# Performance work log

Hardware: AMD Instinct MI355X
Metric: run time of the kernel (lower is better)

The kernel has to match this reference:

```python
import jax, jax.numpy as jnp
import numpy as np

N = 50000      # nodes
E = 800000     # edges
NF = 16        # nfeature_dim
H = 128        # hidden_dim
OUT = 4        # output_dim


def _edge_conv(x, edge_index, W1, b1, W2, b2, aggr):
    """PyG EdgeConv: message = MLP(cat[x_i, x_j - x_i]) per edge, aggregate at target i.
    edge_index[0]=source j, edge_index[1]=target i."""
    src, dst = edge_index[0], edge_index[1]
    xi = x[dst]                                   # [E, F]
    xj = x[src]                                   # [E, F]
    h = jnp.concatenate([xi, xj - xi], axis=-1)   # [E, 2F]
    m = jax.nn.relu(h @ W1 + b1) @ W2 + b2        # [E, H]
    if aggr == 'max':
        out = jax.ops.segment_max(m, dst, num_segments=N)
        out = jnp.where(jnp.isfinite(out), out, 0.0)  # nodes with no in-edges -> 0
    else:  # mean
        s = jax.ops.segment_sum(m, dst, num_segments=N)
        cnt = jax.ops.segment_sum(jnp.ones((m.shape[0], 1), m.dtype), dst, num_segments=N)
        out = s / jnp.maximum(cnt, 1.0)
    return out


def setup_inputs() -> dict:
    key = jax.random.key(0)
    ks = jax.random.split(key, 20)
    s = 0.05
    inp = {
        'x': jax.random.normal(ks[0], (N, NF), dtype=jnp.float32),
        'edge_attr': jax.random.uniform(ks[1], (E, 1), dtype=jnp.float32) + 0.1,
        'edge_index': jax.random.randint(ks[2], (2, E), 0, N, dtype=jnp.int64),
        # conv0: Linear(2*NF->H), Linear(H->H)
        'W01': jax.random.normal(ks[3], (2 * NF, H), dtype=jnp.float32) * s,
        'b01': jnp.zeros((H,), jnp.float32),
        'W02': jax.random.normal(ks[4], (H, H), dtype=jnp.float32) * s,
        'b02': jnp.zeros((H,), jnp.float32),
        # conv1: Linear(2*H->H), Linear(H->H)
        'W11': jax.random.normal(ks[5], (2 * H, H), dtype=jnp.float32) * s,
        'b11': jnp.zeros((H,), jnp.float32),
        'W12': jax.random.normal(ks[6], (H, H), dtype=jnp.float32) * s,
        'b12': jnp.zeros((H,), jnp.float32),
        # conv2: Linear(2*H->H), Linear(H->H)
        'W21': jax.random.normal(ks[7], (2 * H, H), dtype=jnp.float32) * s,
        'b21': jnp.zeros((H,), jnp.float32),
        'W22': jax.random.normal(ks[8], (H, H), dtype=jnp.float32) * s,
        'b22': jnp.zeros((H,), jnp.float32),
        # final fc
        'Wf': jax.random.normal(ks[9], (H, OUT), dtype=jnp.float32) * s,
        'bf': jnp.zeros((OUT,), jnp.float32),
    }
    return inp


def reference(x, edge_attr, edge_index, W01, b01, W02, b02, W11, b11, W12, b12,
              W21, b21, W22, b22, Wf, bf):
    # edge_attr is only nan-checked in the original forward; unused in math.
    # dropout_rate = 0.0 -> identity (eval-mode reference).
    h = _edge_conv(x, edge_index, W01, b01, W02, b02, 'max')
    h = jax.nn.relu(h)
    h = _edge_conv(h, edge_index, W11, b11, W12, b12, 'mean')
    h = jax.nn.relu(h)
    h = _edge_conv(h, edge_index, W21, b21, W22, b22, 'mean')
    return h @ Wf + bf  # [N, OUT]
```

## Files before the change

### kernel.cpp

```cpp
#include <hip/hip_runtime.h>
#include <stdint.h>

#define NNODES 50000
#define NEDGES 800000
#define FDIM 16
#define HDIM 128
#define NPAD 50176
#define NCH 98
#define NBLK64 782

typedef __attribute__((ext_vector_type(8))) short short8;
typedef __attribute__((ext_vector_type(4))) float f32x4;

static constexpr size_t NH  = (size_t)NNODES * HDIM;
static constexpr size_t NHB = NH * sizeof(float);

static constexpr size_t OFF_BUF0  = 0;
static constexpr size_t OFF_BUF1  = NHB;
static constexpr size_t OFF_BUF2  = 2 * NHB;
static constexpr size_t OFF_BFB   = 3 * NHB;
static constexpr size_t OFF_CNT   = OFF_BFB + NH * 2;
static constexpr size_t OFF_CUR   = OFF_CNT + NPAD * 4;
static constexpr size_t OFF_CSUM  = OFF_CUR + NPAD * 4;
static constexpr size_t OFF_COFF  = OFF_CSUM + 512;
static constexpr size_t OFF_WFOLD = OFF_COFF + 512;
static constexpr size_t OFF_BFOLD = OFF_WFOLD + 2048;
static constexpr size_t OFF_FLAG  = OFF_BFOLD + 256;
static constexpr size_t OFF_SEDGE = OFF_FLAG + 256;
static constexpr size_t OFF_W02H  = OFF_SEDGE + (size_t)NEDGES * 8;
static constexpr size_t OFF_W02L  = OFF_W02H + 32768;
static constexpr size_t OFF_W12H  = OFF_W02L + 32768;
static constexpr size_t OFF_W12L  = OFF_W12H + 32768;
static constexpr size_t OFF_W11H  = OFF_W12L + 32768;
static constexpr size_t OFF_W11L  = OFF_W11H + 65536;
static constexpr size_t OFF_W21H  = OFF_W11L + 65536;
static constexpr size_t OFF_W21L  = OFF_W21H + 65536;

__device__ inline unsigned enc_f32(float m) {
  unsigned u = __float_as_uint(m);
  return (u & 0x80000000u) ? ~u : (u | 0x80000000u);
}

__device__ inline ushort bf16_rne(float v) {
  const unsigned u = __float_as_uint(v);
  return (ushort)((u + 0x7fffu + ((u >> 16) & 1u)) >> 16);
}

__device__ inline void bf16_split(float v, ushort& h, ushort& l) {
  unsigned u = __float_as_uint(v);
  unsigned hb = (u + 0x7fffu + ((u >> 16) & 1u)) & 0xffff0000u;
  h = (ushort)(hb >> 16);
  float r = v - __uint_as_float(hb);
  unsigned ur = __float_as_uint(r);
  l = (ushort)((ur + 0x7fffu + ((ur >> 16) & 1u)) >> 16);
}

__device__ inline void split8_tr(const float v[8], short8& hv, short8& lv) {
  unsigned hp[4], lp[4];
  #pragma unroll
  for (int k = 0; k < 4; ++k) {
    const unsigned u0 = __float_as_uint(v[2 * k]);
    const unsigned u1 = __float_as_uint(v[2 * k + 1]);
    const unsigned h0 = u0 & 0xffff0000u;
    const unsigned h1 = u1 & 0xffff0000u;
    const float r0 = v[2 * k]     - __uint_as_float(h0);
    const float r1 = v[2 * k + 1] - __uint_as_float(h1);
    hp[k] = h1 | (h0 >> 16);
    lp[k] = (__float_as_uint(r1) & 0xffff0000u) | (__float_as_uint(r0) >> 16);
  }
  hv = *(short8*)hp;
  lv = *(short8*)lp;
}

__device__ inline short8 cvtpk8_bf16(const float v[8]) {
  unsigned r[4];
  #pragma unroll
  for (int k = 0; k < 4; ++k)
    asm("v_cvt_pk_bf16_f32 %0, %1, %2" : "=v"(r[k]) : "v"(v[2 * k]), "v"(v[2 * k + 1]));
  return *(short8*)r;
}

__global__ __launch_bounds__(256) void k_init(const int* __restrict__ raw,
                                              int* __restrict__ flag,
                                              unsigned* __restrict__ cnt,
                                              unsigned* __restrict__ outenc) {
  const int i = blockIdx.x * 256 + threadIdx.x;
  outenc[i] = 0u;
  if (i < NPAD) cnt[i] = 0u;
  if (i == 0) {
    int is64 = 1;
    #pragma unroll
    for (int k = 1; k < 64; k += 2)
      if (raw[k] != 0) is64 = 0;
    *flag = is64;
  }
}

__global__ __launch_bounds__(256) void k_count(const int* __restrict__ raw,
                                               const int* __restrict__ flag,
                                               unsigned* __restrict__ cnt) {
  const size_t e = (size_t)blockIdx.x * 256 + threadIdx.x;
  const int d = (*flag) ? raw[2 * ((size_t)NEDGES + e)] : raw[NEDGES + e];
  atomicAdd(&cnt[d], 1u);
}

__global__ __launch_bounds__(256) void k_scan1(const unsigned* __restrict__ cnt,
                                               unsigned* __restrict__ csum) {
  __shared__ unsigned s[256];
  const int t = threadIdx.x, b = blockIdx.x;
  s[t] = cnt[b * 512 + t] + cnt[b * 512 + 256 + t];
  __syncthreads();
  for (int off = 128; off; off >>= 1) {
    if (t < off) s[t] += s[t + off];
    __syncthreads();
  }
  if (t == 0) csum[b] = s[0];
}

__global__ void k_scan2(const unsigned* __restrict__ csum,
                        unsigned* __restrict__ coff) {
  if (threadIdx.x == 0) {
    unsigned r = 0;
    for (int i = 0; i < NCH; ++i) { coff[i] = r; r += csum[i]; }
  }
}

__global__ __launch_bounds__(256) void k_scan3(const unsigned* __restrict__ cnt,
                                               const unsigned* __restrict__ coff,
                                               unsigned* __restrict__ cursor) {
  __shared__ unsigned s[256];
  const int t = threadIdx.x, b = blockIdx.x;
  const int base = b * 512;
  const unsigned c0 = cnt[base + 2 * t], c1 = cnt[base + 2 * t + 1];
  s[t] = c0 + c1;
  __syncthreads();
  for (int off = 1; off < 256; off <<= 1) {
    unsigned v = s[t];
    if (t >= off) v += s[t - off];
    __syncthreads();
    s[t] = v;
    __syncthreads();
  }
  const unsigned o = coff[b] + s[t] - (c0 + c1);
  cursor[base + 2 * t] = o;
  cursor[base + 2 * t + 1] = o + c0;
}

__global__ __launch_bounds__(256) void k_scatter(const int* __restrict__ raw,
                                                 const int* __restrict__ flag,
                                                 unsigned* __restrict__ cursor,
                                                 int2* __restrict__ sedge) {
  const size_t e = (size_t)blockIdx.x * 256 + threadIdx.x;
  int s, d;
  if (*flag) { s = raw[2 * e]; d = raw[2 * ((size_t)NEDGES + e)]; }
  else       { s = raw[e];     d = raw[NEDGES + e]; }
  const unsigned p = atomicAdd(&cursor[d], 1u);
  int2 sd; sd.x = s; sd.y = d;
  sedge[p] = sd;
}

__device__ inline void prepw_body(const float* __restrict__ W2,
                                  ushort* __restrict__ Whi,
                                  ushort* __restrict__ Wlo, int blk) {
  const int gid = blk * 256 + threadIdx.x;
  const int row = gid & 15;
  const int kg  = (gid >> 4) & 3;
  const int ks  = (gid >> 6) & 3;
  const int ct  = gid >> 8;
  const int col = ct * 16 + row;
  const int k0  = ks * 32 + kg * 8;
  short8 hv, lv;
  #pragma unroll
  for (int j = 0; j < 8; ++j) {
    ushort h, l;
    bf16_split(W2[(size_t)(k0 + j) * HDIM + col], h, l);
    hv[j] = (short)h; lv[j] = (short)l;
  }
  *(short8*)(Whi + (size_t)gid * 8) = hv;
  *(short8*)(Wlo + (size_t)gid * 8) = lv;
}

__device__ inline void packab_body(const float* __restrict__ W1,
                                   ushort* __restrict__ Whi,
                                   ushort* __restrict__ Wlo, int blk) {
  const int gid = blk * 256 + threadIdx.x;
  const int row = gid & 15;
  const int kg  = (gid >> 4) & 3;
  const int ks  = (gid >> 6) & 3;
  const int ct  = gid >> 8;
  const int col = ct * 16 + row;
  const int k0  = ks * 32 + kg * 8;
  short8 hv, lv;
  #pragma unroll
  for (int j = 0; j < 8; ++j) {
    const int k = k0 + j;
    float v;
    if (col < HDIM) v = W1[(size_t)k * HDIM + col] - W1[(size_t)(k + HDIM) * HDIM + col];
    else            v = W1[(size_t)(k + HDIM) * HDIM + (col - HDIM)];
    ushort h, l;
    bf16_split(v, h, l);
    hv[j] = (short)h; lv[j] = (short)l;
  }
  *(short8*)(Whi + (size_t)gid * 8) = hv;
  *(short8*)(Wlo + (size_t)gid * 8) = lv;
}

__global__ __launch_bounds__(256) void k_prep_all(
    const float* __restrict__ W02, const float* __restrict__ W12,
    const float* __restrict__ W11, const float* __restrict__ W21,
    const float* __restrict__ W22, const float* __restrict__ Wf,
    const float* __restrict__ b22, const float* __restrict__ bf,
    ushort* __restrict__ W02h, ushort* __restrict__ W02l,
    ushort* __restrict__ W12h, ushort* __restrict__ W12l,
    ushort* __restrict__ W11h, ushort* __restrict__ W11l,
    ushort* __restrict__ W21h, ushort* __restrict__ W21l,
    float* __restrict__ Wfold, float* __restrict__ bfold) {
  const int b = blockIdx.x;
  if (b < 8)       prepw_body(W02, W02h, W02l, b);
  else if (b < 16) prepw_body(W12, W12h, W12l, b - 8);
  else if (b < 32) packab_body(W11, W11h, W11l, b - 16);
  else if (b < 48) packab_body(W21, W21h, W21l, b - 32);
  else {
    const int t = (b - 48) * 256 + threadIdx.x;
    const int f = t >> 2, o = t & 3;
    float acc = 0.f;
    for (int h = 0; h < HDIM; ++h)
      acc = fmaf(W22[f * HDIM + h], Wf[h * 4 + o], acc);
    Wfold[t] = acc;
    if (t < 4) {
      float a = bf[t];
      for (int h = 0; h < HDIM; ++h) a = fmaf(b22[h], Wf[h * 4 + t], a);
      bfold[t] = a;
    }
  }
}

__global__ __launch_bounds__(256) void k_node_ab16(const float* __restrict__ x,
                                                   const float* __restrict__ W1,
                                                   const float* __restrict__ b1,
                                                   ushort* __restrict__ Ab,
                                                   ushort* __restrict__ Bb) {
  __shared__ float s_x[16 * FDIM];
  const int tid = threadIdx.x;
  const int nb = blockIdx.x * 16;
  s_x[tid] = x[(size_t)nb * FDIM + tid];
  __syncthreads();
  const int h = tid & 127;
  const int half = tid >> 7;
  float accA[8], accB[8];
  #pragma unroll
  for (int j = 0; j < 8; ++j) { accA[j] = 0.f; accB[j] = 0.f; }
  #pragma unroll 4
  for (int f = 0; f < FDIM; ++f) {
    const float wt = W1[f * HDIM + h];
    const float wb = W1[(f + FDIM) * HDIM + h];
    const float wd = wt - wb;
    #pragma unroll
    for (int j = 0; j < 8; ++j) {
      const float xv = s_x[(half * 8 + j) * FDIM + f];
      accA[j] = fmaf(xv, wd, accA[j]);
      accB[j] = fmaf(xv, wb, accB[j]);
    }
  }
  const float bias = b1[h];
  #pragma unroll
  for (int j = 0; j < 8; ++j) {
    const size_t idx = (size_t)(nb + half * 8 + j) * HDIM + h;
    Ab[idx] = bf16_rne(accA[j] + bias);
    Bb[idx] = bf16_rne(accB[j]);
  }
}

__global__ __launch_bounds__(256) void k_node_ab_mfma(
    const unsigned* __restrict__ X, const ushort* __restrict__ Whi,
    const ushort* __restrict__ Wlo, const float* __restrict__ b1,
    float* __restrict__ A, ushort* __restrict__ Bb) {
  __shared__ __align__(16) ushort s_hi[64 * 128];
  __shared__ __align__(16) ushort s_lo[64 * 128];
  const int tid = threadIdx.x;
  const int nb = blockIdx.x * 64;

  #pragma unroll
  for (int it = 0; it < 4; ++it) {
    const int idx = tid + it * 256;
    const int row = idx >> 4;
    const int kg8 = idx & 15;
    const int n = nb + row;
    float v[8];
    if (n < NNODES) {
      const unsigned* p = X + (size_t)n * HDIM + kg8 * 8;
      const uint4 u0 = *(const uint4*)p;
      const uint4 u1 = *(const uint4*)(p + 4);
      const unsigned uu[8] = {u0.x, u0.y, u0.z, u0.w, u1.x, u1.y, u1.z, u1.w};
      #pragma unroll
      for (int j = 0; j < 8; ++j)
        v[j] = (uu[j] & 0x80000000u) ? __uint_as_float(uu[j] ^ 0x80000000u) : 0.f;
    } else {
      #pragma unroll
      for (int j = 0; j < 8; ++j) v[j] = 0.f;
    }
    short8 hv, lv;
    split8_tr(v, hv, lv);
    const int unit = row * 16 + (kg8 ^ (row & 15));
    *(short8*)(s_hi + unit * 8) = hv;
    *(short8*)(s_lo + unit * 8) = lv;
  }
  __syncthreads();

  const int l15 = tid & 15;
  const int l4  = (tid >> 4) & 3;
  const int w   = tid >> 6;

  f32x4 acc[4][4];
  #pragma unroll
  for (int rt = 0; rt < 4; ++rt)
    #pragma unroll
    for (int c = 0; c < 4; ++c)
      #pragma unroll
      for (int r = 0; r < 4; ++r) acc[rt][c][r] = 0.f;

  #pragma unroll
  for (int ks = 0; ks < 4; ++ks) {
    short8 wh[4], wl[4];
    #pragma unroll
    for (int ctl = 0; ctl < 4; ++ctl) {
      const int ct_g = w * 4 + ctl;
      const size_t u = ((size_t)(((ct_g * 4 + ks) * 4 + l4) * 16 + l15)) * 8;
      wh[ctl] = *(const short8*)(Whi + u);
      wl[ctl] = *(const short8*)(Wlo + u);
    }
    #pragma unroll
    for (int rt = 0; rt < 4; ++rt) {
      const int unit = (rt * 16 + l15) * 16 + ((ks * 4 + l4) ^ l15);
      const short8 ah = *(const short8*)(s_hi + unit * 8);
      const short8 al = *(const short8*)(s_lo + unit * 8);
      #pragma unroll
      for (int ctl = 0; ctl < 4; ++ctl) {
        acc[rt][ctl] = __builtin_amdgcn_mfma_f32_16x16x32_bf16(al, wh[ctl], acc[rt][ctl], 0, 0, 0);
        acc[rt][ctl] = __builtin_amdgcn_mfma_f32_16x16x32_bf16(ah, wl[ctl], acc[rt][ctl], 0, 0, 0);
        acc[rt][ctl] = __builtin_amdgcn_mfma_f32_16x16x32_bf16(ah, wh[ctl], acc[rt][ctl], 0, 0, 0);
      }
    }
  }

  #pragma unroll
  for (int ctl = 0; ctl < 4; ++ctl) {
    const int col_g = w * 64 + ctl * 16 + l15;
    if (col_g < HDIM) {
      const float bias = b1[col_g];
      #pragma unroll
      for (int rt = 0; rt < 4; ++rt)
        #pragma unroll
        for (int r = 0; r < 4; ++r) {
          const int n = nb + rt * 16 + l4 * 4 + r;
          if (n < NNODES) A[(size_t)n * HDIM + col_g] = acc[rt][ctl][r] + bias;
        }
    } else {
      const int cb = col_g - HDIM;
      #pragma unroll
      for (int rt = 0; rt < 4; ++rt)
        #pragma unroll
        for (int r = 0; r < 4; ++r) {
          const int n = nb + rt * 16 + l4 * 4 + r;
          if (n < NNODES) Bb[(size_t)n * HDIM + cb] = bf16_rne(acc[rt][ctl][r]);
        }
    }
  }
}

__global__ __launch_bounds__(256) void k_node_l2_fused(
    const float* __restrict__ S, const unsigned* __restrict__ cnt,
    const ushort* __restrict__ W12h, const ushort* __restrict__ W12l,
    const float* __restrict__ b12,
    const ushort* __restrict__ W21h, const ushort* __restrict__ W21l,
    const float* __restrict__ b21,
    float* __restrict__ A, ushort* __restrict__ Bb) {
  __shared__ __align__(16) ushort s_hi[64 * 128];
  __shared__ __align__(16) ushort s_lo[64 * 128];
  __shared__ float s_m[64 * 132];
  __shared__ float s_scale[64];
  __shared__ float s_alive[64];
  const int tid = threadIdx.x;
  const int nb = blockIdx.x * 64;
  if (tid < 64) {
    const int n = nb + tid;
    const unsigned c = (n < NNODES) ? cnt[n] : 0u;
    s_scale[tid] = c ? 1.f / (float)c : 0.f;
    s_alive[tid] = c ? 1.f : 0.f;
  }
  __syncthreads();

  #pragma unroll
  for (int it = 0; it < 4; ++it) {
    const int idx = tid + it * 256;
    const int row = idx >> 4;
    const int kg8 = idx & 15;
    const int n = nb + row;
    float v[8];
    if (n < NNODES) {
      const float sc = s_scale[row];
      const float* p = S + (size_t)n * HDIM + kg8 * 8;
      const float4 a0 = *(const float4*)p;
      const float4 a1 = *(const float4*)(p + 4);
      v[0] = a0.x * sc; v[1] = a0.y * sc; v[2] = a0.z * sc; v[3] = a0.w * sc;
      v[4] = a1.x * sc; v[5] = a1.y * sc; v[6] = a1.z * sc; v[7] = a1.w * sc;
    } else {
      #pragma unroll
      for (int j = 0; j < 8; ++j) v[j] = 0.f;
    }
    short8 hv, lv;
    split8_tr(v, hv, lv);
    const int unit = row * 16 + (kg8 ^ (row & 15));
    *(short8*)(s_hi + unit * 8) = hv;
    *(short8*)(s_lo + unit * 8) = lv;
  }
  __syncthreads();

  const int l15 = tid & 15;
  const int l4  = (tid >> 4) & 3;
  const int w   = tid >> 6;

  {
    f32x4 acc[4][2];
    #pragma unroll
    for (int rt = 0; rt < 4; ++rt)
      #pragma unroll
      for (int c = 0; c < 2; ++c)
        #pragma unroll
        for (int r = 0; r < 4; ++r) acc[rt][c][r] = 0.f;

    #pragma unroll
    for (int ks = 0; ks < 4; ++ks) {
      short8 wh[2], wl[2];
      #pragma unroll
      for (int ctl = 0; ctl < 2; ++ctl) {
        const int ct_g = w * 2 + ctl;
        const size_t u = ((size_t)(((ct_g * 4 + ks) * 4 + l4) * 16 + l15)) * 8;
        wh[ctl] = *(const short8*)(W12h + u);
        wl[ctl] = *(const short8*)(W12l + u);
      }
      #pragma unroll
      for (int rt = 0; rt < 4; ++rt) {
        const int unit = (rt * 16 + l15) * 16 + ((ks * 4 + l4) ^ l15);
        const short8 ah = *(const short8*)(s_hi + unit * 8);
        const short8 al = *(const short8*)(s_lo + unit * 8);
        #pragma unroll
        for (int ctl = 0; ctl < 2; ++ctl) {
          acc[rt][ctl] = __builtin_amdgcn_mfma_f32_16x16x32_bf16(al, wh[ctl], acc[rt][ctl], 0, 0, 0);
          acc[rt][ctl] = __builtin_amdgcn_mfma_f32_16x16x32_bf16(ah, wl[ctl], acc[rt][ctl], 0, 0, 0);
          acc[rt][ctl] = __builtin_amdgcn_mfma_f32_16x16x32_bf16(ah, wh[ctl], acc[rt][ctl], 0, 0, 0);
        }
      }
    }

    const float bb0 = b12[w * 32 + l15];
    const float bb1 = b12[w * 32 + 16 + l15];
    #pragma unroll
    for (int rt = 0; rt < 4; ++rt)
      #pragma unroll
      for (int ctl = 0; ctl < 2; ++ctl)
        #pragma unroll
        for (int r = 0; r < 4; ++r) {
          const int row = rt * 16 + l4 * 4 + r;
          s_m[row * 132 + w * 32 + ctl * 16 + l15] =
              fmaxf(acc[rt][ctl][r] + (ctl ? bb1 : bb0), 0.f) * s_alive[row];
        }
  }
  __syncthreads();

  #pragma unroll
  for (int it = 0; it < 4; ++it) {
    const int idx = tid + it * 256;
    const int row = idx >> 4;
    const int kg8 = idx & 15;
    const float* p = s_m + row * 132 + kg8 * 8;
    float v[8];
    const float4 a0 = *(const float4*)p;
    const float4 a1 = *(const float4*)(p + 4);
    v[0] = a0.x; v[1] = a0.y; v[2] = a0.z; v[3] = a0.w;
    v[4] = a1.x; v[5] = a1.y; v[6] = a1.z; v[7] = a1.w;
    short8 hv, lv;
    split8_tr(v, hv, lv);
    const int unit = row * 16 + (kg8 ^ (row & 15));
    *(short8*)(s_hi + unit * 8) = hv;
    *(short8*)(s_lo + unit * 8) = lv;
  }
  __syncthreads();

  f32x4 acc2[4][4];
  #pragma unroll
  for (int rt = 0; rt < 4; ++rt)
    #pragma unroll
    for (int c = 0; c < 4; ++c)
      #pragma unroll
      for (int r = 0; r < 4; ++r) acc2[rt][c][r] = 0.f;

  #pragma unroll
  for (int ks = 0; ks < 4; ++ks) {
    short8 wh[4], wl[4];
    #pragma unroll
    for (int ctl = 0; ctl < 4; ++ctl) {
      const int ct_g = w * 4 + ctl;
      const size_t u = ((size_t)(((ct_g * 4 + ks) * 4 + l4) * 16 + l15)) * 8;
      wh[ctl] = *(const short8*)(W21h + u);
      wl[ctl] = *(const short8*)(W21l + u);
    }
    #pragma unroll
    for (int rt = 0; rt < 4; ++rt) {
      const int unit = (rt * 16 + l15) * 16 + ((ks * 4 + l4) ^ l15);
      const short8 ah = *(const short8*)(s_hi + unit * 8);
      const short8 al = *(const short8*)(s_lo + unit * 8);
      #pragma unroll
      for (int ctl = 0; ctl < 4; ++ctl) {
        acc2[rt][ctl] = __builtin_amdgcn_mfma_f32_16x16x32_bf16(al, wh[ctl], acc2[rt][ctl], 0, 0, 0);
        acc2[rt][ctl] = __builtin_amdgcn_mfma_f32_16x16x32_bf16(ah, wl[ctl], acc2[rt][ctl], 0, 0, 0);
        acc2[rt][ctl] = __builtin_amdgcn_mfma_f32_16x16x32_bf16(ah, wh[ctl], acc2[rt][ctl], 0, 0, 0);
      }
    }
  }

  #pragma unroll
  for (int ctl = 0; ctl < 4; ++ctl) {
    const int col_g = w * 64 + ctl * 16 + l15;
    if (col_g < HDIM) {
      const float bias = b21[col_g];
      #pragma unroll
      for (int rt = 0; rt < 4; ++rt)
        #pragma unroll
        for (int r = 0; r < 4; ++r) {
          const int n = nb + rt * 16 + l4 * 4 + r;
          if (n < NNODES) A[(size_t)n * HDIM + col_g] = acc2[rt][ctl][r] + bias;
        }
    } else {
      const int cb = col_g - HDIM;
      #pragma unroll
      for (int rt = 0; rt < 4; ++rt)
        #pragma unroll
        for (int r = 0; r < 4; ++r) {
          const int n = nb + rt * 16 + l4 * 4 + r;
          if (n < NNODES) Bb[(size_t)n * HDIM + cb] = bf16_rne(acc2[rt][ctl][r]);
        }
    }
  }
}

__global__ __launch_bounds__(256) void k_edge_l0_mfma(
    const ushort* __restrict__ A0b, const ushort* __restrict__ B0b,
    const int2* __restrict__ sedge,
    const ushort* __restrict__ Whi,
    const float* __restrict__ b2, unsigned* __restrict__ outenc) {
  __shared__ __align__(16) char s_un[4 * 64 * 17 * 4];
  __shared__ int s_dstA[64];
  __shared__ int s_srcA[64];
  ushort* s_t = (ushort*)s_un;
  float*  s_m = (float*)s_un;

  const int tid = threadIdx.x;
  const int eb = blockIdx.x * 64;
  if (tid < 64) {
    const int2 sd = sedge[eb + tid];
    s_srcA[tid] = sd.x;
    s_dstA[tid] = sd.y;
  }
  __syncthreads();

  #pragma unroll
  for (int it = 0; it < 4; ++it) {
    const int idx = tid + it * 256;
    const int e = idx >> 4;
    const int kg8 = idx & 15;
    const int k0 = kg8 * 8;
    const short8 a8 = *(const short8*)(A0b + (size_t)s_dstA[e] * HDIM + k0);
    const short8 b8 = *(const short8*)(B0b + (size_t)s_srcA[e] * HDIM + k0);
    float v[8];
    #pragma unroll
    for (int j = 0; j < 8; ++j) {
      const float av = __uint_as_float(((unsigned)(ushort)a8[j]) << 16);
      const float bv = __uint_as_float(((unsigned)(ushort)b8[j]) << 16);
      v[j] = fmaxf(av + bv, 0.f);
    }
    const short8 hv = cvtpk8_bf16(v);
    const int unit = e * 16 + (kg8 ^ (e & 15));
    *(short8*)(s_t + unit * 8) = hv;
  }
  __syncthreads();

  const int l15 = tid & 15;
  const int l4  = (tid >> 4) & 3;
  const int w   = tid >> 6;

  f32x4 acc[4][2];
  #pragma unroll
  for (int rt = 0; rt < 4; ++rt)
    #pragma unroll
    for (int c = 0; c < 2; ++c)
      #pragma unroll
      for (int r = 0; r < 4; ++r) acc[rt][c][r] = 0.f;

  #pragma unroll
  for (int ks = 0; ks < 4; ++ks) {
    short8 wh[2];
    #pragma unroll
    for (int ctl = 0; ctl < 2; ++ctl) {
      const int ct_g = w * 2 + ctl;
      const size_t u = ((size_t)(((ct_g * 4 + ks) * 4 + l4) * 16 + l15)) * 8;
      wh[ctl] = *(const short8*)(Whi + u);
    }
    #pragma unroll
    for (int rt = 0; rt < 4; ++rt) {
      const int e = rt * 16 + l15;
      const int unit = e * 16 + ((ks * 4 + l4) ^ l15);
      const short8 ah = *(const short8*)(s_t + unit * 8);
      #pragma unroll
      for (int ctl = 0; ctl < 2; ++ctl)
        acc[rt][ctl] = __builtin_amdgcn_mfma_f32_16x16x32_bf16(ah, wh[ctl], acc[rt][ctl], 0, 0, 0);
    }
  }
  __syncthreads();

  float* smw = s_m + w * (64 * 17);
  const int le = tid & 63;
  const int colw = le & 15;
  const int g = le >> 4;
  const int e0 = g * 16;
  int dd[16];
  #pragma unroll
  for (int e = 0; e < 16; ++e) dd[e] = s_dstA[e0 + e];
  #pragma unroll
  for (int ctl = 0; ctl < 2; ++ctl) {
    const float bb = b2[w * 32 + ctl * 16 + l15];
    #pragma unroll
    for (int rt = 0; rt < 4; ++rt)
      #pragma unroll
      for (int r = 0; r < 4; ++r)
        smw[(rt * 16 + l4 * 4 + r) * 17 + l15] = acc[rt][ctl][r] + bb;
    float vv[16];
    #pragma unroll
    for (int e = 0; e < 16; ++e) vv[e] = smw[(e0 + e) * 17 + colw];
    unsigned* const ocol = outenc + w * 32 + ctl * 16 + colw;
    int curd = dd[0];
    float run = vv[0];
    #pragma unroll
    for (int e = 1; e < 16; ++e) {
      const bool same = (dd[e] == curd);
      if (!same) atomicMax(ocol + (size_t)curd * HDIM, enc_f32(run));
      run = same ? fmaxf(run, vv[e]) : vv[e];
      curd = dd[e];
    }
    atomicMax(ocol + (size_t)curd * HDIM, enc_f32(run));
  }
}

__global__ __launch_bounds__(256) void k_seg_mean(const float* __restrict__ A,
                                                  const ushort* __restrict__ B,
                                                  const int2* __restrict__ sedge,
                                                  const unsigned* __restrict__ endv,
                                                  const unsigned* __restrict__ cnt,
                                                  float* __restrict__ S) {
  const int tid = threadIdx.x;
  const int n = blockIdx.x * 4 + (tid >> 6);
  const int lane = tid & 63;
  const unsigned end = endv[n];
  const unsigned deg = cnt[n];
  const unsigned start = end - deg;
  const float2 a = *(const float2*)(A + (size_t)n * HDIM + lane * 2);
  float sx = 0.f, sy = 0.f;
  for (unsigned cb = start; cb < end; cb += 64) {
    const int m = (int)((end - cb < 64u) ? (end - cb) : 64u);
    int myidx = 0;
    if (lane < m) myidx = sedge[cb + lane].x;
    int k = 0;
    for (; k + 8 <= m; k += 8) {
      unsigned bv[8];
      #pragma unroll
      for (int j = 0; j < 8; ++j) {
        const int id = __shfl(myidx, k + j);
        bv[j] = *(const unsigned*)(B + (size_t)id * HDIM + lane * 2);
      }
      #pragma unroll
      for (int j = 0; j < 8; ++j) {
        sx += fmaxf(a.x + __uint_as_float(bv[j] << 16), 0.f);
        sy += fmaxf(a.y + __uint_as_float(bv[j] & 0xffff0000u), 0.f);
      }
    }
    for (; k < m; ++k) {
      const int id = __shfl(myidx, k);
      const unsigned bv = *(const unsigned*)(B + (size_t)id * HDIM + lane * 2);
      sx += fmaxf(a.x + __uint_as_float(bv << 16), 0.f);
      sy += fmaxf(a.y + __uint_as_float(bv & 0xffff0000u), 0.f);
    }
  }
  float2 o; o.x = sx; o.y = sy;
  *(float2*)(S + (size_t)n * HDIM + lane * 2) = o;
}

__global__ __launch_bounds__(256) void k_seg_final(const float* __restrict__ A,
                                                   const ushort* __restrict__ B,
                                                   const int2* __restrict__ sedge,
                                                   const unsigned* __restrict__ endv,
                                                   const unsigned* __restrict__ cnt,
                                                   const float* __restrict__ Wfold,
                                                   const float* __restrict__ bfold,
                                                   const float* __restrict__ bf,
                                                   float* __restrict__ out) {
  const int tid = threadIdx.x;
  const int n = blockIdx.x * 4 + (tid >> 6);
  const int lane = tid & 63;
  const unsigned deg = cnt[n];
  if (deg == 0) {
    if (lane == 0) {
      float4 o; o.x = bf[0]; o.y = bf[1]; o.z = bf[2]; o.w = bf[3];
      ((float4*)out)[n] = o;
    }
    return;
  }
  const unsigned end = endv[n];
  const unsigned start = end - deg;
  const float2 a = *(const float2*)(A + (size_t)n * HDIM + lane * 2);
  float sx = 0.f, sy = 0.f;
  for (unsigned cb = start; cb < end; cb += 64) {
    const int m = (int)((end - cb < 64u) ? (end - cb) : 64u);
    int myidx = 0;
    if (lane < m) myidx = sedge[cb + lane].x;
    int k = 0;
    for (; k + 8 <= m; k += 8) {
      unsigned bv[8];
      #pragma unroll
      for (int j = 0; j < 8; ++j) {
        const int id = __shfl(myidx, k + j);
        bv[j] = *(const unsigned*)(B + (size_t)id * HDIM + lane * 2);
      }
      #pragma unroll
      for (int j = 0; j < 8; ++j) {
        sx += fmaxf(a.x + __uint_as_float(bv[j] << 16), 0.f);
        sy += fmaxf(a.y + __uint_as_float(bv[j] & 0xffff0000u), 0.f);
      }
    }
    for (; k < m; ++k) {
      const int id = __shfl(myidx, k);
      const unsigned bv = *(const unsigned*)(B + (size_t)id * HDIM + lane * 2);
      sx += fmaxf(a.x + __uint_as_float(bv << 16), 0.f);
      sy += fmaxf(a.y + __uint_as_float(bv & 0xffff0000u), 0.f);
    }
  }
  const float inv = 1.f / (float)deg;
  const float vx = sx * inv, vy = sy * inv;
  const float4 w0 = ((const float4*)Wfold)[lane * 2];
  const float4 w1 = ((const float4*)Wfold)[lane * 2 + 1];
  float p0 = fmaf(vx, w0.x, vy * w1.x);
  float p1 = fmaf(vx, w0.y, vy * w1.y);
  float p2 = fmaf(vx, w0.z, vy * w1.z);
  float p3 = fmaf(vx, w0.w, vy * w1.w);
  #pragma unroll
  for (int off = 32; off; off >>= 1) {
    p0 += __shfl_xor(p0, off);
    p1 += __shfl_xor(p1, off);
    p2 += __shfl_xor(p2, off);
    p3 += __shfl_xor(p3, off);
  }
  if (lane == 0) {
    float4 o;
    o.x = p0 + bfold[0]; o.y = p1 + bfold[1];
    o.z = p2 + bfold[2]; o.w = p3 + bfold[3];
    ((float4*)out)[n] = o;
  }
}

extern "C" void kernel_launch(void* const* d_in, const int* in_sizes, int n_in,
                              void* d_out, int out_size, void* d_ws, size_t ws_size,
                              hipStream_t stream) {
  const float* x   = (const float*)d_in[0];
  const int*   eidx = (const int*)d_in[2];
  const float* W01 = (const float*)d_in[3];
  const float* b01 = (const float*)d_in[4];
  const float* W02 = (const float*)d_in[5];
  const float* b02 = (const float*)d_in[6];
  const float* W11 = (const float*)d_in[7];
  const float* b11 = (const float*)d_in[8];
  const float* W12 = (const float*)d_in[9];
  const float* b12 = (const float*)d_in[10];
  const float* W21 = (const float*)d_in[11];
  const float* b21 = (const float*)d_in[12];
  const float* W22 = (const float*)d_in[13];
  const float* b22 = (const float*)d_in[14];
  const float* Wf  = (const float*)d_in[15];
  const float* bf  = (const float*)d_in[16];
  float* out = (float*)d_out;
  char* ws = (char*)d_ws;

  float* buf0 = (float*)(ws + OFF_BUF0);
  float* buf1 = (float*)(ws + OFF_BUF1);
  float* buf2 = (float*)(ws + OFF_BUF2);
  ushort* bufB = (ushort*)(ws + OFF_BFB);
  unsigned* cnt    = (unsigned*)(ws + OFF_CNT);
  unsigned* cursor = (unsigned*)(ws + OFF_CUR);
  unsigned* csum   = (unsigned*)(ws + OFF_CSUM);
  unsigned* coff   = (unsigned*)(ws + OFF_COFF);
  float* Wfold = (float*)(ws + OFF_WFOLD);
  float* bfold = (float*)(ws + OFF_BFOLD);
  int* flag  = (int*)(ws + OFF_FLAG);
  int2* sedge = (int2*)(ws + OFF_SEDGE);
  ushort* W02h = (ushort*)(ws + OFF_W02H);
  ushort* W02l = (ushort*)(ws + OFF_W02L);
  ushort* W12h = (ushort*)(ws + OFF_W12H);
  ushort* W12l = (ushort*)(ws + OFF_W12L);
  ushort* W11h = (ushort*)(ws + OFF_W11H);
  ushort* W11l = (ushort*)(ws + OFF_W11L);
  ushort* W21h = (ushort*)(ws + OFF_W21H);
  ushort* W21l = (ushort*)(ws + OFF_W21L);

  k_init<<<(int)(NH / 256), 256, 0, stream>>>(eidx, flag, cnt, (unsigned*)buf2);
  k_count<<<NEDGES / 256, 256, 0, stream>>>(eidx, flag, cnt);
  k_scan1<<<NCH, 256, 0, stream>>>(cnt, csum);
  k_scan2<<<1, 64, 0, stream>>>(csum, coff);
  k_scan3<<<NCH, 256, 0, stream>>>(cnt, coff, cursor);
  k_scatter<<<NEDGES / 256, 256, 0, stream>>>(eidx, flag, cursor, sedge);
  k_prep_all<<<50, 256, 0, stream>>>(W02, W12, W11, W21, W22, Wf, b22, bf,
                                     W02h, W02l, W12h, W12l, W11h, W11l,
                                     W21h, W21l, Wfold, bfold);

  ushort* A0b = (ushort*)buf0;
  k_node_ab16<<<NNODES / 16, 256, 0, stream>>>(x, W01, b01, A0b, bufB);
  k_edge_l0_mfma<<<NEDGES / 64, 256, 0, stream>>>(A0b, bufB, sedge,
                                                  W02h, b02, (unsigned*)buf2);

  k_node_ab_mfma<<<NBLK64, 256, 0, stream>>>((const unsigned*)buf2, W11h, W11l,
                                             b11, buf0, bufB);
  k_seg_mean<<<NNODES / 4, 256, 0, stream>>>(buf0, bufB, sedge, cursor, cnt, buf1);

  k_node_l2_fused<<<NBLK64, 256, 0, stream>>>(buf1, cnt, W12h, W12l, b12,
                                              W21h, W21l, b21, buf0, bufB);
  k_seg_final<<<NNODES / 4, 256, 0, stream>>>(buf0, bufB, sedge, cursor, cnt,
                                              Wfold, bfold, bf, out);

  (void)in_sizes; (void)n_in; (void)out_size; (void)ws_size;
}
```

Before: 433.7 us.

## Fuse layer-1 mean aggregation into layer-2 node GEMM and drop activation lo-split

Merges the layer-1 segment-mean gather into the layer-2 node MFMA kernel, so the aggregated features go straight into shared memory as bf16 and the fp32 sum buffer is no longer written and re-read. Activations are now a single bf16 operand instead of a hi/lo split, which removes one of the three MFMAs per tile. The per-node A terms are stored as bf16 instead of fp32, halving that traffic. In exchange, accuracy drops because activations are rounded to plain bf16. The fused kernel also processes 16 nodes per wave serially, which may hurt gather parallelism and latency hiding.

```diff
diff --git a/kernel.cpp b/kernel.cpp
--- a/kernel.cpp
+++ b/kernel.cpp
@@ -15,11 +15,12 @@
 static constexpr size_t NH  = (size_t)NNODES * HDIM;
 static constexpr size_t NHB = NH * sizeof(float);
 
-static constexpr size_t OFF_BUF0  = 0;
-static constexpr size_t OFF_BUF1  = NHB;
-static constexpr size_t OFF_BUF2  = 2 * NHB;
-static constexpr size_t OFF_BFB   = 3 * NHB;
-static constexpr size_t OFF_CNT   = OFF_BFB + NH * 2;
+static constexpr size_t OFF_ENC   = 0;
+static constexpr size_t OFF_PA    = NHB;
+static constexpr size_t OFF_PB    = OFF_PA + NH * 2;
+static constexpr size_t OFF_QA    = OFF_PB + NH * 2;
+static constexpr size_t OFF_QB    = OFF_QA + NH * 2;
+static constexpr size_t OFF_CNT   = OFF_QB + NH * 2;
 static constexpr size_t OFF_CUR   = OFF_CNT + NPAD * 4;
 static constexpr size_t OFF_CSUM  = OFF_CUR + NPAD * 4;
 static constexpr size_t OFF_COFF  = OFF_CSUM + 512;
@@ -55,29 +56,18 @@
   l = (ushort)((ur + 0x7fffu + ((ur >> 16) & 1u)) >> 16);
 }
 
-__device__ inline void split8_tr(const float v[8], short8& hv, short8& lv) {
-  unsigned hp[4], lp[4];
-  #pragma unroll
-  for (int k = 0; k < 4; ++k) {
-    const unsigned u0 = __float_as_uint(v[2 * k]);
-    const unsigned u1 = __float_as_uint(v[2 * k + 1]);
-    const unsigned h0 = u0 & 0xffff0000u;
-    const unsigned h1 = u1 & 0xffff0000u;
-    const float r0 = v[2 * k]     - __uint_as_float(h0);
-    const float r1 = v[2 * k + 1] - __uint_as_float(h1);
-    hp[k] = h1 | (h0 >> 16);
-    lp[k] = (__float_as_uint(r1) & 0xffff0000u) | (__float_as_uint(r0) >> 16);
-  }
-  hv = *(short8*)hp;
-  lv = *(short8*)lp;
-}
-
 __device__ inline short8 cvtpk8_bf16(const float v[8]) {
   unsigned r[4];
   #pragma unroll
   for (int k = 0; k < 4; ++k)
     asm("v_cvt_pk_bf16_f32 %0, %1, %2" : "=v"(r[k]) : "v"(v[2 * k]), "v"(v[2 * k + 1]));
   return *(short8*)r;
+}
+
+__device__ inline unsigned cvtpk_bf16(float a, float b) {
+  unsigned r;
+  asm("v_cvt_pk_bf16_f32 %0, %1, %2" : "=v"(r) : "v"(a), "v"(b));
+  return r;
 }
 
 __global__ __launch_bounds__(256) void k_init(const int* __restrict__ raw,
@@ -274,9 +264,8 @@
 __global__ __launch_bounds__(256) void k_node_ab_mfma(
     const unsigned* __restrict__ X, const ushort* __restrict__ Whi,
     const ushort* __restrict__ Wlo, const float* __restrict__ b1,
-    float* __restrict__ A, ushort* __restrict__ Bb) {
-  __shared__ __align__(16) ushort s_hi[64 * 128];
-  __shared__ __align__(16) ushort s_lo[64 * 128];
+    ushort* __restrict__ Ab, ushort* __restrict__ Bb) {
+  __shared__ __align__(16) ushort s_t[64 * 128];
   const int tid = threadIdx.x;
   const int nb = blockIdx.x * 64;
 
@@ -299,11 +288,9 @@
       #pragma unroll
       for (int j = 0; j < 8; ++j) v[j] = 0.f;
     }
-    short8 hv, lv;
-    split8_tr(v, hv, lv);
+    const short8 hv = cvtpk8_bf16(v);
     const int unit = row * 16 + (kg8 ^ (row & 15));
-    *(short8*)(s_hi + unit * 8) = hv;
-    *(short8*)(s_lo + unit * 8) = lv;
+    *(short8*)(s_t + unit * 8) = hv;
   }
   __syncthreads();
 
@@ -332,11 +319,9 @@
     #pragma unroll
     for (int rt = 0; rt < 4; ++rt) {
       const int unit = (rt * 16 + l15) * 16 + ((ks * 4 + l4) ^ l15);
-      const short8 ah = *(const short8*)(s_hi + unit * 8);
-      const short8 al = *(const short8*)(s_lo + unit * 8);
+      const short8 ah = *(const short8*)(s_t + unit * 8);
       #pragma unroll
       for (int ctl = 0; ctl < 4; ++ctl) {
-        acc[rt][ctl] = __builtin_amdgcn_mfma_f32_16x16x32_bf16(al, wh[ctl], acc[rt][ctl], 0, 0, 0);
         acc[rt][ctl] = __builtin_amdgcn_mfma_f32_16x16x32_bf16(ah, wl[ctl], acc[rt][ctl], 0, 0, 0);
         acc[rt][ctl] = __builtin_amdgcn_mfma_f32_16x16x32_bf16(ah, wh[ctl], acc[rt][ctl], 0, 0, 0);
       }
@@ -353,7 +338,7 @@
         #pragma unroll
         for (int r = 0; r < 4; ++r) {
           const int n = nb + rt * 16 + l4 * 4 + r;
-          if (n < NNODES) A[(size_t)n * HDIM + col_g] = acc[rt][ctl][r] + bias;
+          if (n < NNODES) Ab[(size_t)n * HDIM + col_g] = bf16_rne(acc[rt][ctl][r] + bias);
         }
     } else {
       const int cb = col_g - HDIM;
@@ -368,15 +353,16 @@
   }
 }
 
-__global__ __launch_bounds__(256) void k_node_l2_fused(
-    const float* __restrict__ S, const unsigned* __restrict__ cnt,
+__global__ __launch_bounds__(256) void k_l2_mega(
+    const ushort* __restrict__ A1, const ushort* __restrict__ B1,
+    const int2* __restrict__ sedge, const unsigned* __restrict__ endv,
+    const unsigned* __restrict__ cnt,
     const ushort* __restrict__ W12h, const ushort* __restrict__ W12l,
     const float* __restrict__ b12,
     const ushort* __restrict__ W21h, const ushort* __restrict__ W21l,
     const float* __restrict__ b21,
-    float* __restrict__ A, ushort* __restrict__ Bb) {
-  __shared__ __align__(16) ushort s_hi[64 * 128];
-  __shared__ __align__(16) ushort s_lo[64 * 128];
+    ushort* __restrict__ A2, ushort* __restrict__ B2) {
+  __shared__ __align__(16) ushort s_t[64 * 128];
   __shared__ float s_m[64 * 132];
   __shared__ float s_scale[64];
   __shared__ float s_alive[64];
@@ -390,35 +376,57 @@
   }
   __syncthreads();
 
-  #pragma unroll
-  for (int it = 0; it < 4; ++it) {
-    const int idx = tid + it * 256;
-    const int row = idx >> 4;
-    const int kg8 = idx & 15;
+  const int w    = tid >> 6;
+  const int lane = tid & 63;
+
+  for (int ln = 0; ln < 16; ++ln) {
+    const int row = w * 16 + ln;
     const int n = nb + row;
-    float v[8];
+    float sx = 0.f, sy = 0.f;
+    float ax = 0.f, ay = 0.f;
+    unsigned deg = 0, end = 0;
     if (n < NNODES) {
-      const float sc = s_scale[row];
-      const float* p = S + (size_t)n * HDIM + kg8 * 8;
-      const float4 a0 = *(const float4*)p;
-      const float4 a1 = *(const float4*)(p + 4);
-      v[0] = a0.x * sc; v[1] = a0.y * sc; v[2] = a0.z * sc; v[3] = a0.w * sc;
-      v[4] = a1.x * sc; v[5] = a1.y * sc; v[6] = a1.z * sc; v[7] = a1.w * sc;
-    } else {
-      #pragma unroll
-      for (int j = 0; j < 8; ++j) v[j] = 0.f;
-    }
-    short8 hv, lv;
-    split8_tr(v, hv, lv);
-    const int unit = row * 16 + (kg8 ^ (row & 15));
-    *(short8*)(s_hi + unit * 8) = hv;
-    *(short8*)(s_lo + unit * 8) = lv;
+      deg = cnt[n];
+      end = endv[n];
+      const unsigned a_dw = *(const unsigned*)(A1 + (size_t)n * HDIM + lane * 2);
+      ax = __uint_as_float(a_dw << 16);
+      ay = __uint_as_float(a_dw & 0xffff0000u);
+    }
+    const unsigned start = end - deg;
+    for (unsigned cb = start; cb < end; cb += 64) {
+      const int m = (int)((end - cb < 64u) ? (end - cb) : 64u);
+      int myidx = 0;
+      if (lane < m) myidx = sedge[cb + lane].x;
+      int k = 0;
+      for (; k + 8 <= m; k += 8) {
+        unsigned bv[8];
+        #pragma unroll
+        for (int j = 0; j < 8; ++j) {
+          const int id = __shfl(myidx, k + j);
+          bv[j] = *(const unsigned*)(B1 + (size_t)id * HDIM + lane * 2);
+        }
+        #pragma unroll
+        for (int j = 0; j < 8; ++j) {
+          sx += fmaxf(ax + __uint_as_float(bv[j] << 16), 0.f);
+          sy += fmaxf(ay + __uint_as_float(bv[j] & 0xffff0000u), 0.f);
+        }
+      }
+      for (; k < m; ++k) {
+        const int id = __shfl(myidx, k);
+        const unsigned bv = *(const unsigned*)(B1 + (size_t)id * HDIM + lane * 2);
+        sx += fmaxf(ax + __uint_as_float(bv << 16), 0.f);
+        sy += fmaxf(ay + __uint_as_float(bv & 0xffff0000u), 0.f);
+      }
+    }
+    const float sc = s_scale[row];
+    const unsigned pk = cvtpk_bf16(sx * sc, sy * sc);
+    const int unit = row * 16 + ((lane >> 2) ^ (row & 15));
+    *(unsigned*)((char*)s_t + unit * 16 + (lane & 3) * 4) = pk;
   }
   __syncthreads();
 
   const int l15 = tid & 15;
   const int l4  = (tid >> 4) & 3;
-  const int w   = tid >> 6;
 
   {
     f32x4 acc[4][2];
@@ -442,11 +450,9 @@
       #pragma unroll
       for (int rt = 0; rt < 4; ++rt) {
         const int unit = (rt * 16 + l15) * 16 + ((ks * 4 + l4) ^ l15);
-        const short8 ah = *(const short8*)(s_hi + unit * 8);
-        const short8 al = *(const short8*)(s_lo + unit * 8);
+        const short8 ah = *(const short8*)(s_t + unit * 8);
         #pragma unroll
         for (int ctl = 0; ctl < 2; ++ctl) {
-          acc[rt][ctl] = __builtin_amdgcn_mfma_f32_16x16x32_bf16(al, wh[ctl], acc[rt][ctl], 0, 0, 0);
           acc[rt][ctl] = __builtin_amdgcn_mfma_f32_16x16x32_bf16(ah, wl[ctl], acc[rt][ctl], 0, 0, 0);
           acc[rt][ctl] = __builtin_amdgcn_mfma_f32_16x16x32_bf16(ah, wh[ctl], acc[rt][ctl], 0, 0, 0);
         }
@@ -479,11 +485,9 @@
     const float4 a1 = *(const float4*)(p + 4);
     v[0] = a0.x; v[1] = a0.y; v[2] = a0.z; v[3] = a0.w;
     v[4] = a1.x; v[5] = a1.y; v[6] = a1.z; v[7] = a1.w;
-    short8 hv, lv;
-    split8_tr(v, hv, lv);
+    const short8 hv = cvtpk8_bf16(v);
     const int unit = row * 16 + (kg8 ^ (row & 15));
-    *(short8*)(s_hi + unit * 8) = hv;
-    *(short8*)(s_lo + unit * 8) = lv;
+    *(short8*)(s_t + unit * 8) = hv;
   }
   __syncthreads();
 
@@ -508,11 +512,9 @@
     #pragma unroll
     for (int rt = 0; rt < 4; ++rt) {
       const int unit = (rt * 16 + l15) * 16 + ((ks * 4 + l4) ^ l15);
-      const short8 ah = *(const short8*)(s_hi + unit * 8);
-      const short8 al = *(const short8*)(s_lo + unit * 8);
+      const short8 ah = *(const short8*)(s_t + unit * 8);
       #pragma unroll
       for (int ctl = 0; ctl < 4; ++ctl) {
-        acc2[rt][ctl] = __builtin_amdgcn_mfma_f32_16x16x32_bf16(al, wh[ctl], acc2[rt][ctl], 0, 0, 0);
         acc2[rt][ctl] = __builtin_amdgcn_mfma_f32_16x16x32_bf16(ah, wl[ctl], acc2[rt][ctl], 0, 0, 0);
         acc2[rt][ctl] = __builtin_amdgcn_mfma_f32_16x16x32_bf16(ah, wh[ctl], acc2[rt][ctl], 0, 0, 0);
       }
@@ -529,7 +531,7 @@
         #pragma unroll
         for (int r = 0; r < 4; ++r) {
           const int n = nb + rt * 16 + l4 * 4 + r;
-          if (n < NNODES) A[(size_t)n * HDIM + col_g] = acc2[rt][ctl][r] + bias;
+          if (n < NNODES) A2[(size_t)n * HDIM + col_g] = bf16_rne(acc2[rt][ctl][r] + bias);
         }
     } else {
       const int cb = col_g - HDIM;
@@ -538,7 +540,7 @@
         #pragma unroll
         for (int r = 0; r < 4; ++r) {
           const int n = nb + rt * 16 + l4 * 4 + r;
-          if (n < NNODES) Bb[(size_t)n * HDIM + cb] = bf16_rne(acc2[rt][ctl][r]);
+          if (n < NNODES) B2[(size_t)n * HDIM + cb] = bf16_rne(acc2[rt][ctl][r]);
         }
     }
   }
@@ -651,50 +653,7 @@
   }
 }
 
-__global__ __launch_bounds__(256) void k_seg_mean(const float* __restrict__ A,
-                                                  const ushort* __restrict__ B,
-                                                  const int2* __restrict__ sedge,
-                                                  const unsigned* __restrict__ endv,
-                                                  const unsigned* __restrict__ cnt,
-                                                  float* __restrict__ S) {
-  const int tid = threadIdx.x;
-  const int n = blockIdx.x * 4 + (tid >> 6);
-  const int lane = tid & 63;
-  const unsigned end = endv[n];
-  const unsigned deg = cnt[n];
-  const unsigned start = end - deg;
-  const float2 a = *(const float2*)(A + (size_t)n * HDIM + lane * 2);
-  float sx = 0.f, sy = 0.f;
-  for (unsigned cb = start; cb < end; cb += 64) {
-    const int m = (int)((end - cb < 64u) ? (end - cb) : 64u);
-    int myidx = 0;
-    if (lane < m) myidx = sedge[cb + lane].x;
-    int k = 0;
-    for (; k + 8 <= m; k += 8) {
-      unsigned bv[8];
-      #pragma unroll
-      for (int j = 0; j < 8; ++j) {
-        const int id = __shfl(myidx, k + j);
-        bv[j] = *(const unsigned*)(B + (size_t)id * HDIM + lane * 2);
-      }
-      #pragma unroll
-      for (int j = 0; j < 8; ++j) {
-        sx += fmaxf(a.x + __uint_as_float(bv[j] << 16), 0.f);
-        sy += fmaxf(a.y + __uint_as_float(bv[j] & 0xffff0000u), 0.f);
-      }
-    }
-    for (; k < m; ++k) {
-      const int id = __shfl(myidx, k);
-      const unsigned bv = *(const unsigned*)(B + (size_t)id * HDIM + lane * 2);
-      sx += fmaxf(a.x + __uint_as_float(bv << 16), 0.f);
-      sy += fmaxf(a.y + __uint_as_float(bv & 0xffff0000u), 0.f);
-    }
-  }
-  float2 o; o.x = sx; o.y = sy;
-  *(float2*)(S + (size_t)n * HDIM + lane * 2) = o;
-}
-
-__global__ __launch_bounds__(256) void k_seg_final(const float* __restrict__ A,
+__global__ __launch_bounds__(256) void k_seg_final(const ushort* __restrict__ A,
                                                    const ushort* __restrict__ B,
                                                    const int2* __restrict__ sedge,
                                                    const unsigned* __restrict__ endv,
@@ -716,7 +675,9 @@
   }
   const unsigned end = endv[n];
   const unsigned start = end - deg;
-  const float2 a = *(const float2*)(A + (size_t)n * HDIM + lane * 2);
+  const unsigned a_dw = *(const unsigned*)(A + (size_t)n * HDIM + lane * 2);
+  const float ax = __uint_as_float(a_dw << 16);
+  const float ay = __uint_as_float(a_dw & 0xffff0000u);
   float sx = 0.f, sy = 0.f;
   for (unsigned cb = start; cb < end; cb += 64) {
     const int m = (int)((end - cb < 64u) ? (end - cb) : 64u);
@@ -732,15 +693,15 @@
       }
       #pragma unroll
       for (int j = 0; j < 8; ++j) {
-        sx += fmaxf(a.x + __uint_as_float(bv[j] << 16), 0.f);
-        sy += fmaxf(a.y + __uint_as_float(bv[j] & 0xffff0000u), 0.f);
+        sx += fmaxf(ax + __uint_as_float(bv[j] << 16), 0.f);
+        sy += fmaxf(ay + __uint_as_float(bv[j] & 0xffff0000u), 0.f);
       }
     }
     for (; k < m; ++k) {
       const int id = __shfl(myidx, k);
       const unsigned bv = *(const unsigned*)(B + (size_t)id * HDIM + lane * 2);
-      sx += fmaxf(a.x + __uint_as_float(bv << 16), 0.f);
-      sy += fmaxf(a.y + __uint_as_float(bv & 0xffff0000u), 0.f);
+      sx += fmaxf(ax + __uint_as_float(bv << 16), 0.f);
+      sy += fmaxf(ay + __uint_as_float(bv & 0xffff0000u), 0.f);
     }
   }
   const float inv = 1.f / (float)deg;
@@ -788,10 +749,11 @@
   float* out = (float*)d_out;
   char* ws = (char*)d_ws;
 
-  float* buf0 = (float*)(ws + OFF_BUF0);
-  float* buf1 = (float*)(ws + OFF_BUF1);
-  float* buf2 = (float*)(ws + OFF_BUF2);
-  ushort* bufB = (ushort*)(ws + OFF_BFB);
+  unsigned* enc = (unsigned*)(ws + OFF_ENC);
+  ushort* PA = (ushort*)(ws + OFF_PA);
+  ushort* PB = (ushort*)(ws + OFF_PB);
+  ushort* QA = (ushort*)(ws + OFF_QA);
+  ushort* QB = (ushort*)(ws + OFF_QB);
   unsigned* cnt    = (unsigned*)(ws + OFF_CNT);
   unsigned* cursor = (unsigned*)(ws + OFF_CUR);
   unsigned* csum   = (unsigned*)(ws + OFF_CSUM);
@@ -809,7 +771,7 @@
   ushort* W21h = (ushort*)(ws + OFF_W21H);
   ushort* W21l = (ushort*)(ws + OFF_W21L);
 
-  k_init<<<(int)(NH / 256), 256, 0, stream>>>(eidx, flag, cnt, (unsigned*)buf2);
+  k_init<<<(int)(NH / 256), 256, 0, stream>>>(eidx, flag, cnt, enc);
   k_count<<<NEDGES / 256, 256, 0, stream>>>(eidx, flag, cnt);
   k_scan1<<<NCH, 256, 0, stream>>>(cnt, csum);
   k_scan2<<<1, 64, 0, stream>>>(csum, coff);
@@ -819,18 +781,16 @@
                                      W02h, W02l, W12h, W12l, W11h, W11l,
                                      W21h, W21l, Wfold, bfold);
 
-  ushort* A0b = (ushort*)buf0;
-  k_node_ab16<<<NNODES / 16, 256, 0, stream>>>(x, W01, b01, A0b, bufB);
-  k_edge_l0_mfma<<<NEDGES / 64, 256, 0, stream>>>(A0b, bufB, sedge,
-                                                  W02h, b02, (unsigned*)buf2);
-
-  k_node_ab_mfma<<<NBLK64, 256, 0, stream>>>((const unsigned*)buf2, W11h, W11l,
-                                             b11, buf0, bufB);
-  k_seg_mean<<<NNODES / 4, 256, 0, stream>>>(buf0, bufB, sedge, cursor, cnt, buf1);
-
-  k_node_l2_fused<<<NBLK64, 256, 0, stream>>>(buf1, cnt, W12h, W12l, b12,
-                                              W21h, W21l, b21, buf0, bufB);
-  k_seg_final<<<NNODES / 4, 256, 0, stream>>>(buf0, bufB, sedge, cursor, cnt,
+  k_node_ab16<<<NNODES / 16, 256, 0, stream>>>(x, W01, b01, PA, PB);
+  k_edge_l0_mfma<<<NEDGES / 64, 256, 0, stream>>>(PA, PB, sedge, W02h, b02, enc);
+
+  k_node_ab_mfma<<<NBLK64, 256, 0, stream>>>(enc, W11h, W11l, b11, QA, QB);
+
+  k_l2_mega<<<NBLK64, 256, 0, stream>>>(QA, QB, sedge, cursor, cnt,
+                                        W12h, W12l, b12, W21h, W21l, b21,
+                                        PA, PB);
+
+  k_seg_final<<<NNODES / 4, 256, 0, stream>>>(PA, PB, sedge, cursor, cnt,
                                               Wfold, bfold, bf, out);
 
   (void)in_sizes; (void)n_in; (void)out_size; (void)ws_size;
```

Result: slower. 476.5 us (+9.9%).
